# Kernel optimization log

Hardware: AMD Instinct MI355X
Metric: run time of the kernel (lower is better)

## Reference

```python
import jax, jax.numpy as jnp
import numpy as np

# Grouped TF->gene sparse decoder dims
T = 512       # number of TFs (tf_size)
K = 4         # nodes_per_tf (width_multiplier); decoder_features = T*K = 2048
G = 20000     # number of genes (gene_size)
EPG = 3       # regulating TFs per gene (TF-gene edges per gene)
B = 512       # batch of cells


def setup_inputs() -> dict:
    key = jax.random.key(0)
    k0, k1, k2, k3, k4, k5, k6 = jax.random.split(key, 7)
    features = jax.random.normal(k0, (B, T), dtype=jnp.float32)
    # Layer 1: each TF fans out to its own K hidden nodes (one weight per edge)
    w1 = jax.random.normal(k1, (T, K), dtype=jnp.float32) * 0.5
    b1 = jax.random.normal(k2, (T, K), dtype=jnp.float32) * 0.1
    # Layer 2: block-dense KxK mixing within each TF group
    w2 = jax.random.normal(k3, (T, K, K), dtype=jnp.float32) * (1.0 / np.sqrt(K))
    b2 = jax.random.normal(k4, (T, K), dtype=jnp.float32) * 0.1
    # Output layer: gene g sums over its EPG TF edges x K hidden nodes
    w3 = jax.random.normal(k5, (G, EPG, K), dtype=jnp.float32) * (1.0 / np.sqrt(EPG * K))
    b3 = jax.random.normal(k6, (G,), dtype=jnp.float32) * 0.1
    # Fixed irregular TF-gene connectivity (constant structure, like data_obj)
    edge_tf = jnp.asarray(
        np.random.default_rng(0).integers(0, T, size=(G, EPG)), dtype=jnp.int32
    )
    return {"features": features, "w1": w1, "b1": b1, "w2": w2, "b2": b2,
            "w3": w3, "b3": b3, "edge_tf": edge_tf}


def reference(features, w1, b1, w2, b2, w3, b3, edge_tf):
    # SparseLinear decoder_1: TF t -> its K hidden nodes, then LeakyReLU(0.01)
    h1 = jax.nn.leaky_relu(features[:, :, None] * w1 + b1)            # [B,T,K]
    # SparseLinear decoder_2: block-dense within each TF group + LeakyReLU
    h2 = jax.nn.leaky_relu(jnp.einsum('btj,tjk->btk', h1, w2) + b2)   # [B,T,K]
    # SparseLinear output: gather each gene's regulating TF groups, contract
    gathered = h2[:, edge_tf, :]                                      # [B,G,EPG,K]
    out = jnp.einsum('bgek,gek->bg', gathered, w3) + b3               # [B,G]
    return out
```

## Files before the change

kernel.cpp:

```cpp
#include <hip/hip_runtime.h>

namespace {

constexpr int T = 512;
constexpr int K = 4;
constexpr int G = 20000;
constexpr int EPG = 3;
constexpr int B = 512;
constexpr int BT = 2;
constexpr int NSLAB = B / BT;
constexpr int NG = 6;
constexpr int GPB = 3584;
constexpr int NCHUNK = GPB / 256;
constexpr int GPAD = NG * GPB;
constexpr int RS = 12;
constexpr float SLOPE = 0.01f;

__device__ __forceinline__ float lrelu(float x) { return fmaxf(x, SLOPE * x); }
__device__ __forceinline__ float dot4(float4 a, float4 b) {
  return a.x * b.x + a.y * b.y + a.z * b.z + a.w * b.w;
}

__global__ __launch_bounds__(256) void prep_kernel(
    const float* __restrict__ w3, const float* __restrict__ b3,
    const int* __restrict__ edge, float4* __restrict__ R0,
    float4* __restrict__ R1, float4* __restrict__ R2, float4* __restrict__ RM) {
  const int g = blockIdx.x * 256 + threadIdx.x;
  float4 a = make_float4(0.f, 0.f, 0.f, 0.f), b = a, c = a, m = a;
  if (g < G) {
    const float4* wp = reinterpret_cast<const float4*>(w3 + (size_t)g * (EPG * K));
    a = wp[0];
    b = wp[1];
    c = wp[2];
    m.x = b3[g];
    m.y = __int_as_float(edge[g * EPG + 0] * (RS * 4));
    m.z = __int_as_float(edge[g * EPG + 1] * (RS * 4));
    m.w = __int_as_float(edge[g * EPG + 2] * (RS * 4));
  } else {
    m.y = m.z = m.w = __int_as_float(0);
  }
  R0[g] = a; R1[g] = b; R2[g] = c; RM[g] = m;
}

__global__ __launch_bounds__(256, 8) void fused_kernel(
    const float* __restrict__ features, const float* __restrict__ w1,
    const float* __restrict__ b1, const float* __restrict__ w2,
    const float* __restrict__ b2, const float4* __restrict__ R0,
    const float4* __restrict__ R1, const float4* __restrict__ R2,
    const float4* __restrict__ RM, float* __restrict__ out) {
  __shared__ float lds[T * RS];
  const int tid = threadIdx.x;
  const int b0 = blockIdx.x * BT;
  const int gbase = blockIdx.y * GPB;

#pragma unroll
  for (int half = 0; half < 2; ++half) {
    const int t = half * 256 + tid;
    const float4 W1 = reinterpret_cast<const float4*>(w1)[t];
    const float4 B1 = reinterpret_cast<const float4*>(b1)[t];
    const float4 B2 = reinterpret_cast<const float4*>(b2)[t];
    const float4* W2 = reinterpret_cast<const float4*>(w2) + t * 4;
    const float4 r0 = W2[0];
    const float4 r1 = W2[1];
    const float4 r2 = W2[2];
    const float4 r3 = W2[3];
#pragma unroll
    for (int b = 0; b < BT; ++b) {
      const float f = features[(size_t)(b0 + b) * T + t];
      const float h0 = lrelu(f * W1.x + B1.x);
      const float h1 = lrelu(f * W1.y + B1.y);
      const float h2 = lrelu(f * W1.z + B1.z);
      const float h3 = lrelu(f * W1.w + B1.w);
      float4 o;
      o.x = lrelu(B2.x + h0 * r0.x + h1 * r1.x + h2 * r2.x + h3 * r3.x);
      o.y = lrelu(B2.y + h0 * r0.y + h1 * r1.y + h2 * r2.y + h3 * r3.y);
      o.z = lrelu(B2.z + h0 * r0.z + h1 * r1.z + h2 * r2.z + h3 * r3.z);
      o.w = lrelu(B2.w + h0 * r0.w + h1 * r1.w + h2 * r2.w + h3 * r3.w);
      *reinterpret_cast<float4*>(&lds[t * RS + b * 4]) = o;
    }
  }
  __syncthreads();

  const char* ldsc = reinterpret_cast<const char*>(lds);

  for (int s = 0; s < NCHUNK; ++s) {
    const int g = gbase + s * 256 + tid;
    const float4 c0 = R0[g];
    const float4 c1 = R1[g];
    const float4 c2 = R2[g];
    const float4 cm = RM[g];
    const int o0 = __float_as_int(cm.y);
    const int o1 = __float_as_int(cm.z);
    const int o2 = __float_as_int(cm.w);
    float a0 = cm.x, a1 = cm.x;
    {
      const float4 v0 = *reinterpret_cast<const float4*>(ldsc + o0);
      const float4 v1 = *reinterpret_cast<const float4*>(ldsc + o0 + 16);
      a0 += dot4(v0, c0);
      a1 += dot4(v1, c0);
    }
    {
      const float4 v0 = *reinterpret_cast<const float4*>(ldsc + o1);
      const float4 v1 = *reinterpret_cast<const float4*>(ldsc + o1 + 16);
      a0 += dot4(v0, c1);
      a1 += dot4(v1, c1);
    }
    {
      const float4 v0 = *reinterpret_cast<const float4*>(ldsc + o2);
      const float4 v1 = *reinterpret_cast<const float4*>(ldsc + o2 + 16);
      a0 += dot4(v0, c2);
      a1 += dot4(v1, c2);
    }
    if (g < G) {
      __builtin_nontemporal_store(a0, &out[(size_t)(b0 + 0) * G + g]);
      __builtin_nontemporal_store(a1, &out[(size_t)(b0 + 1) * G + g]);
    }
  }
}

}

extern "C" void kernel_launch(void* const* d_in, const int* in_sizes, int n_in,
                              void* d_out, int out_size, void* d_ws, size_t ws_size,
                              hipStream_t stream) {
  const float* features = (const float*)d_in[0];
  const float* w1 = (const float*)d_in[1];
  const float* b1 = (const float*)d_in[2];
  const float* w2 = (const float*)d_in[3];
  const float* b2 = (const float*)d_in[4];
  const float* w3 = (const float*)d_in[5];
  const float* b3 = (const float*)d_in[6];
  const int* edge = (const int*)d_in[7];
  float* out = (float*)d_out;

  float4* R0 = (float4*)d_ws;
  float4* R1 = R0 + GPAD;
  float4* R2 = R1 + GPAD;
  float4* RM = R2 + GPAD;

  prep_kernel<<<GPAD / 256, 256, 0, stream>>>(w3, b3, edge, R0, R1, R2, RM);

  dim3 grid(NSLAB, NG);
  fused_kernel<<<grid, 256, 0, stream>>>(features, w1, b1, w2, b2, R0, R1, R2,
                                         RM, out);
}
```

Baseline: 97.27 us.

## Process 8 batch rows per block with swizzled LDS and prefetched gene weights

Raises the batch rows per block from 2 to 8 and changes the thread mapping so each thread handles one batch row for one gene, with 32 genes per chunk. The h2 table in LDS is widened to 8 rows per TF with an XOR-style rotation to spread bank accesses. The next chunk's gene weights are software-prefetched into registers. Weight traffic per output drops because each gene's weights are reused across 8 rows. In exchange, LDS use grows to 64KB, which caps occupancy at about 2 blocks per CU, and output stores become 8 separate row segments of 32 floats. The nontemporal stores are replaced by plain stores.

```diff
diff --git a/kernel.cpp b/kernel.cpp
--- a/kernel.cpp
+++ b/kernel.cpp
@@ -7,13 +7,13 @@
 constexpr int G = 20000;
 constexpr int EPG = 3;
 constexpr int B = 512;
-constexpr int BT = 2;
+constexpr int BT = 8;
 constexpr int NSLAB = B / BT;
-constexpr int NG = 6;
-constexpr int GPB = 3584;
-constexpr int NCHUNK = GPB / 256;
+constexpr int NG = 8;
+constexpr int CH = 32;
+constexpr int NCHUNK = 79;
+constexpr int GPB = NCHUNK * CH;
 constexpr int GPAD = NG * GPB;
-constexpr int RS = 12;
 constexpr float SLOPE = 0.01f;
 
 __device__ __forceinline__ float lrelu(float x) { return fmaxf(x, SLOPE * x); }
@@ -33,22 +33,22 @@
     b = wp[1];
     c = wp[2];
     m.x = b3[g];
-    m.y = __int_as_float(edge[g * EPG + 0] * (RS * 4));
-    m.z = __int_as_float(edge[g * EPG + 1] * (RS * 4));
-    m.w = __int_as_float(edge[g * EPG + 2] * (RS * 4));
+    m.y = __int_as_float(edge[g * EPG + 0]);
+    m.z = __int_as_float(edge[g * EPG + 1]);
+    m.w = __int_as_float(edge[g * EPG + 2]);
   } else {
     m.y = m.z = m.w = __int_as_float(0);
   }
   R0[g] = a; R1[g] = b; R2[g] = c; RM[g] = m;
 }
 
-__global__ __launch_bounds__(256, 8) void fused_kernel(
+__global__ __launch_bounds__(256, 2) void fused_kernel(
     const float* __restrict__ features, const float* __restrict__ w1,
     const float* __restrict__ b1, const float* __restrict__ w2,
     const float* __restrict__ b2, const float4* __restrict__ R0,
     const float4* __restrict__ R1, const float4* __restrict__ R2,
     const float4* __restrict__ RM, float* __restrict__ out) {
-  __shared__ float lds[T * RS];
+  __shared__ float lds[T * 32];
   const int tid = threadIdx.x;
   const int b0 = blockIdx.x * BT;
   const int gbase = blockIdx.y * GPB;
@@ -76,45 +76,39 @@
       o.y = lrelu(B2.y + h0 * r0.y + h1 * r1.y + h2 * r2.y + h3 * r3.y);
       o.z = lrelu(B2.z + h0 * r0.z + h1 * r1.z + h2 * r2.z + h3 * r3.z);
       o.w = lrelu(B2.w + h0 * r0.w + h1 * r1.w + h2 * r2.w + h3 * r3.w);
-      *reinterpret_cast<float4*>(&lds[t * RS + b * 4]) = o;
+      const int sw = ((b + t) & 7) * 4;
+      *reinterpret_cast<float4*>(&lds[t * 32 + sw]) = o;
     }
   }
   __syncthreads();
 
   const char* ldsc = reinterpret_cast<const char*>(lds);
+  const int b = tid & 7;
+  const int gsub = tid >> 3;
 
+  float4 pw0, pw1, pw2, pm;
+  {
+    const int g = gbase + gsub;
+    pw0 = R0[g]; pw1 = R1[g]; pw2 = R2[g]; pm = RM[g];
+  }
   for (int s = 0; s < NCHUNK; ++s) {
-    const int g = gbase + s * 256 + tid;
-    const float4 c0 = R0[g];
-    const float4 c1 = R1[g];
-    const float4 c2 = R2[g];
-    const float4 cm = RM[g];
-    const int o0 = __float_as_int(cm.y);
-    const int o1 = __float_as_int(cm.z);
-    const int o2 = __float_as_int(cm.w);
-    float a0 = cm.x, a1 = cm.x;
-    {
-      const float4 v0 = *reinterpret_cast<const float4*>(ldsc + o0);
-      const float4 v1 = *reinterpret_cast<const float4*>(ldsc + o0 + 16);
-      a0 += dot4(v0, c0);
-      a1 += dot4(v1, c0);
+    const float4 c0 = pw0, c1 = pw1, c2 = pw2, cm = pm;
+    const int g = gbase + s * CH + gsub;
+    if (s + 1 < NCHUNK) {
+      const int gn = gbase + (s + 1) * CH + gsub;
+      pw0 = R0[gn]; pw1 = R1[gn]; pw2 = R2[gn]; pm = RM[gn];
     }
-    {
-      const float4 v0 = *reinterpret_cast<const float4*>(ldsc + o1);
-      const float4 v1 = *reinterpret_cast<const float4*>(ldsc + o1 + 16);
-      a0 += dot4(v0, c1);
-      a1 += dot4(v1, c1);
-    }
-    {
-      const float4 v0 = *reinterpret_cast<const float4*>(ldsc + o2);
-      const float4 v1 = *reinterpret_cast<const float4*>(ldsc + o2 + 16);
-      a0 += dot4(v0, c2);
-      a1 += dot4(v1, c2);
-    }
-    if (g < G) {
-      __builtin_nontemporal_store(a0, &out[(size_t)(b0 + 0) * G + g]);
-      __builtin_nontemporal_store(a1, &out[(size_t)(b0 + 1) * G + g]);
-    }
+    const int t0 = __float_as_int(cm.y);
+    const int t1 = __float_as_int(cm.z);
+    const int t2 = __float_as_int(cm.w);
+    const float4 v0 = *reinterpret_cast<const float4*>(
+        ldsc + (t0 << 7) + (((b + t0) & 7) << 4));
+    const float4 v1 = *reinterpret_cast<const float4*>(
+        ldsc + (t1 << 7) + (((b + t1) & 7) << 4));
+    const float4 v2 = *reinterpret_cast<const float4*>(
+        ldsc + (t2 << 7) + (((b + t2) & 7) << 4));
+    const float a = cm.x + dot4(v0, c0) + dot4(v1, c1) + dot4(v2, c2);
+    if (g < G) out[(size_t)(b0 + b) * G + g] = a;
   }
 }
 
```

Result: slower. 113.5 us (+16.7%).
